# Kernel tuning notes

Hardware: AMD Instinct MI355X
Metric: run time of the kernel (lower is better)

Reference implementation:

```python
import jax, jax.numpy as jnp
import numpy as np

B, F_IN, NCH, T = 1, 1, 1536, 128
NW = [476, 476, 292]          # wires per plane (face 0)
NC = [10000, 10000, 10000]    # crossings per plane pair (01, 12, 20)
NCROSS = sum(NC)
E = 120000                    # ~4 nearest-neighbor edges per crossing node
N_FEAT_WIRE = 4
OUT_CH = 4
NODE_DIM = 2 * (F_IN + N_FEAT_WIRE) + 3  # = 13, matches GAT input dim


def setup_inputs() -> dict:
    key = jax.random.key(0)
    ks = jax.random.split(key, 18)
    x = jax.random.normal(ks[0], (B, F_IN, NCH, T), jnp.float32)
    chan_p0 = jax.random.randint(ks[1], (NW[0],), 0, NCH, jnp.int32)
    chan_p1 = jax.random.randint(ks[2], (NW[1],), 0, NCH, jnp.int32)
    chan_p2 = jax.random.randint(ks[3], (NW[2],), 0, NCH, jnp.int32)
    gidx_01 = jax.random.randint(ks[4], (NC[0], 2), 0, min(NW[0], NW[1]), jnp.int32)
    gidx_12 = jax.random.randint(ks[5], (NC[1], 2), 0, min(NW[1], NW[2]), jnp.int32)
    gidx_20 = jax.random.randint(ks[6], (NC[2], 2), 0, min(NW[2], NW[0]), jnp.int32)
    ray_01 = jax.random.normal(ks[7], (NC[0], 2), jnp.float32)
    ray_12 = jax.random.normal(ks[8], (NC[1], 2), jnp.float32)
    ray_20 = jax.random.normal(ks[9], (NC[2], 2), jnp.float32)
    edges = jax.random.randint(ks[10], (2, E), 0, NCROSS, jnp.int32)
    W_gat = jax.random.normal(ks[11], (NODE_DIM, OUT_CH), jnp.float32) * 0.1
    a_src = jax.random.normal(ks[12], (OUT_CH,), jnp.float32) * 0.1
    a_dst = jax.random.normal(ks[13], (OUT_CH,), jnp.float32) * 0.1
    b_gat = jnp.zeros((OUT_CH,), jnp.float32)
    W_mlp = jax.random.normal(ks[14], (OUT_CH, 1), jnp.float32) * 0.1
    b_mlp = jnp.zeros((1,), jnp.float32)
    return dict(x=x, chan_p0=chan_p0, chan_p1=chan_p1, chan_p2=chan_p2,
                gidx_01=gidx_01, gidx_12=gidx_12, gidx_20=gidx_20,
                ray_01=ray_01, ray_12=ray_12, ray_20=ray_20, edges=edges,
                W_gat=W_gat, a_src=a_src, a_dst=a_dst, b_gat=b_gat,
                W_mlp=W_mlp, b_mlp=b_mlp)


def _plane_feats(x, chan, plane_id):
    # x: [B,F,C,T] -> per-wire features [B,T,Nw,F+4]:
    # (signal, wire_ident, channel, 0, plane_id) -- mirrors as_wires_f0_pX.
    sig = jnp.transpose(x[:, :, chan, :], (0, 3, 2, 1))  # [B,T,Nw,F]
    nw = chan.shape[0]
    wire_id = jnp.arange(nw, dtype=jnp.float32)
    extra = jnp.stack([wire_id, chan.astype(jnp.float32),
                       jnp.zeros(nw, jnp.float32),
                       jnp.full((nw,), plane_id, jnp.float32)], axis=-1)  # [Nw,4]
    extra = jnp.broadcast_to(extra[None, None], sig.shape[:2] + extra.shape)
    return jnp.concatenate([sig, extra], axis=-1)


def _cross(fA, fB, gidx, rc):
    # crossing node features: wireA feats ++ wireB feats ++ ray xy ++ tick
    n = gidx.shape[0]
    tick = jnp.broadcast_to(jnp.arange(T, dtype=jnp.float32)[None, :, None, None],
                            (B, T, n, 1))
    rcb = jnp.broadcast_to(rc[None, None], (B, T, n, 2))
    return jnp.concatenate([fA[:, :, gidx[:, 0]], fB[:, :, gidx[:, 1]], rcb, tick],
                           axis=-1)  # [B,T,n,13]


def _gat_one(h, a_src, a_dst, src, dst):
    # single-graph, single-head GAT attention + aggregation. h: [N,OUT_CH]
    s = h @ a_src  # [N]
    d = h @ a_dst
    e = jax.nn.leaky_relu(s[src] + d[dst], 0.2)  # [E]
    m = jax.ops.segment_max(e, dst, num_segments=NCROSS)
    m = jnp.where(jnp.isfinite(m), m, 0.0)
    w = jnp.exp(e - m[dst])
    denom = jax.ops.segment_sum(w, dst, num_segments=NCROSS)
    msg = jax.ops.segment_sum(w[:, None] * h[src], dst, num_segments=NCROSS)
    return msg / (denom[:, None] + 1e-9)


def reference(x, chan_p0, chan_p1, chan_p2, gidx_01, gidx_12, gidx_20,
              ray_01, ray_12, ray_20, edges,
              W_gat, a_src, a_dst, b_gat, W_mlp, b_mlp):
    f0 = _plane_feats(x, chan_p0, 0.0)
    f1 = _plane_feats(x, chan_p1, 1.0)
    f2 = _plane_feats(x, chan_p2, 2.0)
    nodes = jnp.concatenate([_cross(f0, f1, gidx_01, ray_01),
                             _cross(f1, f2, gidx_12, ray_12),
                             _cross(f2, f0, gidx_20, ray_20)], axis=2)  # [B,T,N,13]
    h = nodes @ W_gat + b_gat  # [B,T,N,OUT_CH]
    src, dst = edges[0], edges[1]
    gat = jax.vmap(jax.vmap(lambda hh: _gat_one(hh, a_src, a_dst, src, dst)))
    g = gat(h)  # [B,T,N,OUT_CH]
    return jax.nn.sigmoid(g @ W_mlp + b_mlp)  # [B,T,N,1]
```

## Files before the change

### kernel.cpp

```cpp
#include <hip/hip_runtime.h>

#define T_TICKS 128
#define NCHAN   1536
#define NCPAIR  10000
#define NCROSS  30000
#define E_EDGES 120000
#define TG      4
#define NTG     (T_TICKS / TG)
#define NBLK_N  ((NCROSS + 255) / 256)
#define CAP     24
#define EPB     ((E_EDGES + NBLK_N - 1) / NBLK_N)


__global__ void k_prep(const float* __restrict__ x,
                       const int* __restrict__ c0, const int* __restrict__ c1,
                       const int* __restrict__ c2,
                       const int* __restrict__ g01, const int* __restrict__ g12,
                       const int* __restrict__ g20,
                       const float* __restrict__ r01,
                       const float* __restrict__ r12,
                       const float* __restrict__ r20,
                       const float* __restrict__ Wg,
                       const float* __restrict__ bg,
                       const float* __restrict__ as_,
                       const float* __restrict__ ad_,
                       const float* __restrict__ Wm,
                       const int* __restrict__ e_src,
                       const int* __restrict__ e_dst,
                       int* __restrict__ counts,
                       unsigned short* __restrict__ bucket,
                       float4* __restrict__ crec) {
    const int tid = threadIdx.x;
    {
        const int lo = blockIdx.x * EPB;
        const int hi = min(lo + EPB, E_EDGES);
        for (int i = lo + tid; i < hi; i += 256) {
            const int s = e_src[i];
            const int d = e_dst[i];
            const int slot = atomicAdd(&counts[d], 1);
            if (slot < CAP) bucket[(size_t)d * CAP + slot] = (unsigned short)s;
        }
    }
    const int n = blockIdx.x * 256 + tid;
    if (n >= NCROSS) return;

    int iA, iB, m;
    float pA, pB;
    const int* cA;
    const int* cB;
    const float* ray;
    if (n < NCPAIR) {
        m = n; cA = c0; cB = c1; pA = 0.f; pB = 1.f; ray = r01;
        iA = g01[2 * m]; iB = g01[2 * m + 1];
    } else if (n < 2 * NCPAIR) {
        m = n - NCPAIR; cA = c1; cB = c2; pA = 1.f; pB = 2.f; ray = r12;
        iA = g12[2 * m]; iB = g12[2 * m + 1];
    } else {
        m = n - 2 * NCPAIR; cA = c2; cB = c0; pA = 2.f; pB = 0.f; ray = r20;
        iA = g20[2 * m]; iB = g20[2 * m + 1];
    }
    const int chA = cA[iA];
    const int chB = cB[iB];
    const float rx = ray[2 * m];
    const float ry = ray[2 * m + 1];

    float base[4];
#pragma unroll
    for (int c = 0; c < 4; c++) {
        base[c] = bg[c]
                + (float)iA  * Wg[1 * 4 + c] + (float)chA * Wg[2 * 4 + c]
                + pA         * Wg[4 * 4 + c]
                + (float)iB  * Wg[6 * 4 + c] + (float)chB * Wg[7 * 4 + c]
                + pB         * Wg[9 * 4 + c]
                + rx         * Wg[10 * 4 + c] + ry * Wg[11 * 4 + c];
    }
    float sB = 0, dB = 0, pBs = 0;
    float sA1 = 0, dA1 = 0, pA1 = 0;
    float sB1 = 0, dB1 = 0, pB1 = 0;
    float sT = 0, dT = 0, pT = 0;
#pragma unroll
    for (int c = 0; c < 4; c++) {
        const float va = as_[c], vd = ad_[c], vm = Wm[c];
        sB  += base[c] * va;  dB  += base[c] * vd;  pBs += base[c] * vm;
        sA1 += Wg[c] * va;    dA1 += Wg[c] * vd;    pA1 += Wg[c] * vm;
        sB1 += Wg[5*4+c]*va;  dB1 += Wg[5*4+c]*vd;  pB1 += Wg[5*4+c]*vm;
        sT  += Wg[12*4+c]*va; dT  += Wg[12*4+c]*vd; pT  += Wg[12*4+c]*vm;
    }
    crec[(size_t)n * 4 + 0] = make_float4(sB, sA1, sB1, sT);
    crec[(size_t)n * 4 + 1] = make_float4(pBs, pA1, pB1, pT);
    crec[(size_t)n * 4 + 2] = make_float4(dB, dA1, dB1, dT);
    crec[(size_t)n * 4 + 3] = make_float4(__int_as_float(chA),
                                          __int_as_float(chB), 0.f, 0.f);
}


__device__ __forceinline__ void upd(float& mx, float& den, float& p,
                                    const float e, const float pj) {
    const float dif = e - mx;
    const float ex = __expf(-fabsf(dif));
    const bool g = dif > 0.f;
    const float scale = g ? ex : 1.f;
    const float w = g ? 1.f : ex;
    mx = g ? e : mx;
    den = fmaf(den, scale, w);
    p = fmaf(p, scale, w * pj);
}

__global__ void k_gat(const float4* __restrict__ crec,
                      const float* __restrict__ x,
                      const int* __restrict__ counts,
                      const unsigned short* __restrict__ bucket,
                      const float* __restrict__ bm,
                      float* __restrict__ out) {
    const int nb = blockIdx.x;
    const int tg = blockIdx.y;
    const int t0 = tg * TG;
    const float t0f = (float)t0;
    const int bbase = nb * 256;
    const int tid = threadIdx.x;
    const int wsz = min(256, NCROSS - bbase);

    __shared__ float4 xt[NCHAN];
    __shared__ int perm[256];
    __shared__ int bins[CAP + 1];
    __shared__ int boff[CAP + 1];
    __shared__ float lres[TG][257];

    for (int c = tid; c < NCHAN; c += 256)
        xt[c] = *(const float4*)(x + c * T_TICKS + t0);

    int deg0 = 0;
    if (tid < wsz) deg0 = min(counts[bbase + tid], CAP);
    if (tid <= CAP) bins[tid] = 0;
    __syncthreads();
    int lp = 0;
    if (tid < wsz) lp = atomicAdd(&bins[deg0], 1);
    __syncthreads();
    if (tid == 0) {
        int run = 0;
        for (int d = CAP; d >= 0; d--) { boff[d] = run; run += bins[d]; }
    }
    __syncthreads();
    if (tid < wsz) perm[boff[deg0] + lp] = tid;
    __syncthreads();

    if (tid < wsz) {
        const int nloc = perm[tid];
        const int n = bbase + nloc;
        const int deg = min(counts[n], CAP);
        const unsigned short* bkt = bucket + (size_t)n * CAP;

        float dd[TG];
        {
            const float4 cd = crec[(size_t)n * 4 + 2];
            const float4 cq = crec[(size_t)n * 4 + 3];
            const float4 xa = xt[__float_as_int(cq.x)];
            const float4 xb = xt[__float_as_int(cq.y)];
            const float sa[4] = {xa.x, xa.y, xa.z, xa.w};
            const float sb[4] = {xb.x, xb.y, xb.z, xb.w};
            float dbase = fmaf(t0f, cd.w, cd.x);
#pragma unroll
            for (int k = 0; k < TG; k++) {
                dd[k] = fmaf(sa[k], cd.y, fmaf(sb[k], cd.z, dbase));
                dbase += cd.w;
            }
        }

        float mx[TG], den[TG], pa[TG];
#pragma unroll
        for (int k = 0; k < TG; k++) { mx[k] = -INFINITY; den[k] = 0.f; pa[k] = 0.f; }

        auto visit = [&](const int src) {
            const float4 ca = crec[(size_t)src * 4 + 0];
            const float4 cp = crec[(size_t)src * 4 + 1];
            const float4 cq = crec[(size_t)src * 4 + 3];
            const float4 xa = xt[__float_as_int(cq.x)];
            const float4 xb = xt[__float_as_int(cq.y)];
            const float sa[4] = {xa.x, xa.y, xa.z, xa.w};
            const float sb[4] = {xb.x, xb.y, xb.z, xb.w};
            float sbase = fmaf(t0f, ca.w, ca.x);
            float pbase = fmaf(t0f, cp.w, cp.x);
#pragma unroll
            for (int k = 0; k < TG; k++) {
                float e = fmaf(sa[k], ca.y, fmaf(sb[k], ca.z, sbase)) + dd[k];
                e = fmaxf(e, 0.2f * e);
                const float pj = fmaf(sa[k], cp.y, fmaf(sb[k], cp.z, pbase));
                upd(mx[k], den[k], pa[k], e, pj);
                sbase += ca.w;
                pbase += cp.w;
            }
        };

        int j = 0;
        for (; j + 2 <= deg; j += 2) {
            const int s0 = bkt[j];
            const int s1 = bkt[j + 1];
            visit(s0);
            visit(s1);
        }
        if (j < deg) visit(bkt[j]);

        const float bb = bm[0];
#pragma unroll
        for (int k = 0; k < TG; k++) {
            const float logit = pa[k] / (den[k] + 1e-9f) + bb;
            lres[k][nloc] = 1.f / (1.f + __expf(-logit));
        }
    }
    __syncthreads();
    if (tid < wsz) {
#pragma unroll
        for (int k = 0; k < TG; k++) {
            out[(size_t)(t0 + k) * NCROSS + bbase + tid] = lres[k][tid];
        }
    }
}


extern "C" void kernel_launch(void* const* d_in, const int* in_sizes, int n_in,
                              void* d_out, int out_size, void* d_ws, size_t ws_size,
                              hipStream_t stream) {
    const float* x   = (const float*)d_in[0];
    const int* c0  = (const int*)d_in[1];
    const int* c1  = (const int*)d_in[2];
    const int* c2  = (const int*)d_in[3];
    const int* g01 = (const int*)d_in[4];
    const int* g12 = (const int*)d_in[5];
    const int* g20 = (const int*)d_in[6];
    const float* r01 = (const float*)d_in[7];
    const float* r12 = (const float*)d_in[8];
    const float* r20 = (const float*)d_in[9];
    const int* edges = (const int*)d_in[10];
    const float* Wg  = (const float*)d_in[11];
    const float* as_ = (const float*)d_in[12];
    const float* ad_ = (const float*)d_in[13];
    const float* bg  = (const float*)d_in[14];
    const float* Wm  = (const float*)d_in[15];
    const float* bm  = (const float*)d_in[16];
    float* out = (float*)d_out;

    const int* e_src = edges;
    const int* e_dst = edges + E_EDGES;

    char* ws = (char*)d_ws;
    size_t off = 0;
    int* counts            = (int*)(ws + off);            off += NCROSS * sizeof(int);
    off = (off + 63) & ~(size_t)63;
    unsigned short* bucket = (unsigned short*)(ws + off); off += (size_t)NCROSS * CAP * 2;
    off = (off + 63) & ~(size_t)63;
    float4* crec           = (float4*)(ws + off);         off += (size_t)NCROSS * 64;
    (void)ws_size; (void)n_in; (void)in_sizes; (void)out_size;

    hipMemsetAsync(counts, 0, NCROSS * sizeof(int), stream);

    k_prep<<<NBLK_N, 256, 0, stream>>>(x, c0, c1, c2, g01, g12, g20,
                                       r01, r12, r20, Wg, bg, as_, ad_, Wm,
                                       e_src, e_dst, counts, bucket, crec);
    dim3 gridG(NBLK_N, NTG);
    k_gat<<<gridG, 256, 0, stream>>>(crec, x, counts, bucket, bm, out);
}
```

Baseline: 153.5 us.

## Precompute per-tick source scores in prep kernel and remap GAT blocks per XCD

The prep kernel now runs over a 2D grid, one slice per tick group, and writes each node's source attention score and projection for 8 ticks into a tick-group-major buffer. The GAT kernel no longer stages x into shared memory or rebuilds per-source values from gathered channel data. Each edge visit becomes a 64-byte contiguous load followed by the online softmax update. Tick groups double to 8 and the launch becomes 1D, with block indices remapped so tick groups spread across the XCDs. In exchange the workspace grows to about 30 MB of extra writes and reads, and register pressure rises with TG=8.

```diff
diff --git a/kernel.cpp b/kernel.cpp
--- a/kernel.cpp
+++ b/kernel.cpp
@@ -5,14 +5,14 @@
 #define NCPAIR  10000
 #define NCROSS  30000
 #define E_EDGES 120000
-#define TG      4
+#define TG      8
 #define NTG     (T_TICKS / TG)
 #define NBLK_N  ((NCROSS + 255) / 256)
 #define CAP     24
 #define EPB     ((E_EDGES + NBLK_N - 1) / NBLK_N)
 
 
-__global__ void k_prep(const float* __restrict__ x,
+__global__ void k_feat(const float* __restrict__ x,
                        const int* __restrict__ c0, const int* __restrict__ c1,
                        const int* __restrict__ c2,
                        const int* __restrict__ g01, const int* __restrict__ g12,
@@ -29,9 +29,10 @@
                        const int* __restrict__ e_dst,
                        int* __restrict__ counts,
                        unsigned short* __restrict__ bucket,
-                       float4* __restrict__ crec) {
+                       float4* __restrict__ sp4, float4* __restrict__ dc4) {
     const int tid = threadIdx.x;
-    {
+    const int tg = blockIdx.y;
+    if (tg == 0) {
         const int lo = blockIdx.x * EPB;
         const int hi = min(lo + EPB, E_EDGES);
         for (int i = lo + tid; i < hi; i += 256) {
@@ -86,11 +87,31 @@
         sB1 += Wg[5*4+c]*va;  dB1 += Wg[5*4+c]*vd;  pB1 += Wg[5*4+c]*vm;
         sT  += Wg[12*4+c]*va; dT  += Wg[12*4+c]*vd; pT  += Wg[12*4+c]*vm;
     }
-    crec[(size_t)n * 4 + 0] = make_float4(sB, sA1, sB1, sT);
-    crec[(size_t)n * 4 + 1] = make_float4(pBs, pA1, pB1, pT);
-    crec[(size_t)n * 4 + 2] = make_float4(dB, dA1, dB1, dT);
-    crec[(size_t)n * 4 + 3] = make_float4(__int_as_float(chA),
-                                          __int_as_float(chB), 0.f, 0.f);
+    if (tg == 0) {
+        dc4[(size_t)n * 2]     = make_float4(dB, dA1, dB1, dT);
+        dc4[(size_t)n * 2 + 1] = make_float4(__int_as_float(chA),
+                                             __int_as_float(chB), 0.f, 0.f);
+    }
+
+    const int t0 = tg * TG;
+    const float4 xa0 = *(const float4*)(x + chA * T_TICKS + t0);
+    const float4 xa1 = *(const float4*)(x + chA * T_TICKS + t0 + 4);
+    const float4 xb0 = *(const float4*)(x + chB * T_TICKS + t0);
+    const float4 xb1 = *(const float4*)(x + chB * T_TICKS + t0 + 4);
+    const float sa[8] = {xa0.x, xa0.y, xa0.z, xa0.w, xa1.x, xa1.y, xa1.z, xa1.w};
+    const float sb[8] = {xb0.x, xb0.y, xb0.z, xb0.w, xb1.x, xb1.y, xb1.z, xb1.w};
+    float sv[8], pv[8];
+#pragma unroll
+    for (int k = 0; k < TG; k++) {
+        const float tk = (float)(t0 + k);
+        sv[k] = sB  + sa[k] * sA1 + sb[k] * sB1 + tk * sT;
+        pv[k] = pBs + sa[k] * pA1 + sb[k] * pB1 + tk * pT;
+    }
+    float4* rec = sp4 + ((size_t)tg * NCROSS + n) * 4;
+    rec[0] = make_float4(sv[0], pv[0], sv[1], pv[1]);
+    rec[1] = make_float4(sv[2], pv[2], sv[3], pv[3]);
+    rec[2] = make_float4(sv[4], pv[4], sv[5], pv[5]);
+    rec[3] = make_float4(sv[6], pv[6], sv[7], pv[7]);
 }
 
 
@@ -106,28 +127,28 @@
     p = fmaf(p, scale, w * pj);
 }
 
-__global__ void k_gat(const float4* __restrict__ crec,
+__global__ void k_gat(const float4* __restrict__ sp4,
+                      const float4* __restrict__ dc4,
                       const float* __restrict__ x,
                       const int* __restrict__ counts,
                       const unsigned short* __restrict__ bucket,
                       const float* __restrict__ bm,
                       float* __restrict__ out) {
-    const int nb = blockIdx.x;
-    const int tg = blockIdx.y;
-    const int t0 = tg * TG;
-    const float t0f = (float)t0;
+    const int lid = blockIdx.x;
+    const int xcd = lid & 7;
+    const int s   = lid >> 3;
+    const int q   = s / NBLK_N;
+    const int nb  = s - q * NBLK_N;
+    const int tg  = xcd + 8 * q;
+    const int t0  = tg * TG;
     const int bbase = nb * 256;
     const int tid = threadIdx.x;
     const int wsz = min(256, NCROSS - bbase);
 
-    __shared__ float4 xt[NCHAN];
     __shared__ int perm[256];
     __shared__ int bins[CAP + 1];
     __shared__ int boff[CAP + 1];
     __shared__ float lres[TG][257];
-
-    for (int c = tid; c < NCHAN; c += 256)
-        xt[c] = *(const float4*)(x + c * T_TICKS + t0);
 
     int deg0 = 0;
     if (tid < wsz) deg0 = min(counts[bbase + tid], CAP);
@@ -152,13 +173,19 @@
 
         float dd[TG];
         {
-            const float4 cd = crec[(size_t)n * 4 + 2];
-            const float4 cq = crec[(size_t)n * 4 + 3];
-            const float4 xa = xt[__float_as_int(cq.x)];
-            const float4 xb = xt[__float_as_int(cq.y)];
-            const float sa[4] = {xa.x, xa.y, xa.z, xa.w};
-            const float sb[4] = {xb.x, xb.y, xb.z, xb.w};
-            float dbase = fmaf(t0f, cd.w, cd.x);
+            const float4 cd = dc4[(size_t)n * 2];
+            const float4 cq = dc4[(size_t)n * 2 + 1];
+            const int chA = __float_as_int(cq.x);
+            const int chB = __float_as_int(cq.y);
+            const float4 xa0 = *(const float4*)(x + chA * T_TICKS + t0);
+            const float4 xa1 = *(const float4*)(x + chA * T_TICKS + t0 + 4);
+            const float4 xb0 = *(const float4*)(x + chB * T_TICKS + t0);
+            const float4 xb1 = *(const float4*)(x + chB * T_TICKS + t0 + 4);
+            const float sa[8] = {xa0.x, xa0.y, xa0.z, xa0.w,
+                                 xa1.x, xa1.y, xa1.z, xa1.w};
+            const float sb[8] = {xb0.x, xb0.y, xb0.z, xb0.w,
+                                 xb1.x, xb1.y, xb1.z, xb1.w};
+            float dbase = fmaf((float)t0, cd.w, cd.x);
 #pragma unroll
             for (int k = 0; k < TG; k++) {
                 dd[k] = fmaf(sa[k], cd.y, fmaf(sb[k], cd.z, dbase));
@@ -170,35 +197,34 @@
 #pragma unroll
         for (int k = 0; k < TG; k++) { mx[k] = -INFINITY; den[k] = 0.f; pa[k] = 0.f; }
 
-        auto visit = [&](const int src) {
-            const float4 ca = crec[(size_t)src * 4 + 0];
-            const float4 cp = crec[(size_t)src * 4 + 1];
-            const float4 cq = crec[(size_t)src * 4 + 3];
-            const float4 xa = xt[__float_as_int(cq.x)];
-            const float4 xb = xt[__float_as_int(cq.y)];
-            const float sa[4] = {xa.x, xa.y, xa.z, xa.w};
-            const float sb[4] = {xb.x, xb.y, xb.z, xb.w};
-            float sbase = fmaf(t0f, ca.w, ca.x);
-            float pbase = fmaf(t0f, cp.w, cp.x);
-#pragma unroll
-            for (int k = 0; k < TG; k++) {
-                float e = fmaf(sa[k], ca.y, fmaf(sb[k], ca.z, sbase)) + dd[k];
-                e = fmaxf(e, 0.2f * e);
-                const float pj = fmaf(sa[k], cp.y, fmaf(sb[k], cp.z, pbase));
-                upd(mx[k], den[k], pa[k], e, pj);
-                sbase += ca.w;
-                pbase += cp.w;
-            }
+        const float4* spb = sp4 + (size_t)tg * NCROSS * 4;
+
+        auto visit = [&](const float4 f0, const float4 f1,
+                         const float4 f2, const float4 f3) {
+            float e;
+            e = f0.x + dd[0]; e = fmaxf(e, 0.2f * e); upd(mx[0], den[0], pa[0], e, f0.y);
+            e = f0.z + dd[1]; e = fmaxf(e, 0.2f * e); upd(mx[1], den[1], pa[1], e, f0.w);
+            e = f1.x + dd[2]; e = fmaxf(e, 0.2f * e); upd(mx[2], den[2], pa[2], e, f1.y);
+            e = f1.z + dd[3]; e = fmaxf(e, 0.2f * e); upd(mx[3], den[3], pa[3], e, f1.w);
+            e = f2.x + dd[4]; e = fmaxf(e, 0.2f * e); upd(mx[4], den[4], pa[4], e, f2.y);
+            e = f2.z + dd[5]; e = fmaxf(e, 0.2f * e); upd(mx[5], den[5], pa[5], e, f2.w);
+            e = f3.x + dd[6]; e = fmaxf(e, 0.2f * e); upd(mx[6], den[6], pa[6], e, f3.y);
+            e = f3.z + dd[7]; e = fmaxf(e, 0.2f * e); upd(mx[7], den[7], pa[7], e, f3.w);
         };
 
         int j = 0;
         for (; j + 2 <= deg; j += 2) {
-            const int s0 = bkt[j];
-            const int s1 = bkt[j + 1];
-            visit(s0);
-            visit(s1);
-        }
-        if (j < deg) visit(bkt[j]);
+            const float4* r0 = spb + (size_t)bkt[j] * 4;
+            const float4* r1 = spb + (size_t)bkt[j + 1] * 4;
+            const float4 a0 = r0[0], a1 = r0[1], a2 = r0[2], a3 = r0[3];
+            const float4 b0 = r1[0], b1 = r1[1], b2 = r1[2], b3 = r1[3];
+            visit(a0, a1, a2, a3);
+            visit(b0, b1, b2, b3);
+        }
+        if (j < deg) {
+            const float4* r0 = spb + (size_t)bkt[j] * 4;
+            visit(r0[0], r0[1], r0[2], r0[3]);
+        }
 
         const float bb = bm[0];
 #pragma unroll
@@ -248,14 +274,16 @@
     off = (off + 63) & ~(size_t)63;
     unsigned short* bucket = (unsigned short*)(ws + off); off += (size_t)NCROSS * CAP * 2;
     off = (off + 63) & ~(size_t)63;
-    float4* crec           = (float4*)(ws + off);         off += (size_t)NCROSS * 64;
+    float4* dc4            = (float4*)(ws + off);         off += (size_t)NCROSS * 32;
+    off = (off + 255) & ~(size_t)255;
+    float4* sp4            = (float4*)(ws + off);         off += (size_t)NTG * NCROSS * 64;
     (void)ws_size; (void)n_in; (void)in_sizes; (void)out_size;
 
     hipMemsetAsync(counts, 0, NCROSS * sizeof(int), stream);
 
-    k_prep<<<NBLK_N, 256, 0, stream>>>(x, c0, c1, c2, g01, g12, g20,
-                                       r01, r12, r20, Wg, bg, as_, ad_, Wm,
-                                       e_src, e_dst, counts, bucket, crec);
-    dim3 gridG(NBLK_N, NTG);
-    k_gat<<<gridG, 256, 0, stream>>>(crec, x, counts, bucket, bm, out);
-}
+    dim3 gridF(NBLK_N, NTG);
+    k_feat<<<gridF, 256, 0, stream>>>(x, c0, c1, c2, g01, g12, g20,
+                                      r01, r12, r20, Wg, bg, as_, ad_, Wm,
+                                      e_src, e_dst, counts, bucket, sp4, dc4);
+    k_gat<<<NBLK_N * NTG, 256, 0, stream>>>(sp4, dc4, x, counts, bucket, bm, out);
+}
```

New measurement: 155.7 us. About the same (+1.4%).
